# Performance work log

Hardware: AMD Instinct MI355X
Metric: run time of the kernel (lower is better)

Reference implementation:

```python
import jax, jax.numpy as jnp
import numpy as np

N = 50000
D = 256
S = 25  # num_samples


def setup_inputs() -> dict:
    key = jax.random.key(0)
    ks = jax.random.split(key, 8)
    sc = 1.0 / np.sqrt(D)
    sc2 = 1.0 / np.sqrt(2 * D)
    return {
        "features": jax.random.normal(ks[0], (N, D), dtype=jnp.float32),
        "neigh_idx": jax.random.randint(ks[1], (N, S), 0, N, dtype=jnp.int64),
        "Wp0": jax.random.normal(ks[2], (D, D), dtype=jnp.float32) * sc,
        "bp0": jnp.zeros((D,), dtype=jnp.float32),
        "Wfc0": jax.random.normal(ks[3], (2 * D, D), dtype=jnp.float32) * sc2,
        "bfc0": jnp.zeros((D,), dtype=jnp.float32),
        "Wp1": jax.random.normal(ks[4], (D, D), dtype=jnp.float32) * sc,
        "bp1": jnp.zeros((D,), dtype=jnp.float32),
        "Wfc1": jax.random.normal(ks[5], (2 * D, D), dtype=jnp.float32) * sc2,
        "bfc1": jnp.zeros((D,), dtype=jnp.float32),
    }


def _sage_layer(out, neigh_idx, Wp, bp, Wfc, bfc):
    # MaxPoolAggregator: per-node Linear+ReLU on neighbor feats, then max-pool.
    # Transform once over all nodes, then gather (same math, less traffic).
    h = jax.nn.relu(out @ Wp + bp)          # [N, d]
    agg = jnp.max(h[neigh_idx], axis=1)     # gather [N, S, d] -> max -> [N, d]
    cat = jnp.concatenate([out, agg], axis=1)  # [N, 2d]
    return cat @ Wfc + bfc                  # [N, hidden]


def reference(features, neigh_idx, Wp0, bp0, Wfc0, bfc0, Wp1, bp1, Wfc1, bfc1):
    out = _sage_layer(features, neigh_idx, Wp0, bp0, Wfc0, bfc0)
    out = jax.nn.relu(out)  # relu between layers; dropout(p=0) is a no-op
    out = _sage_layer(out, neigh_idx, Wp1, bp1, Wfc1, bfc1)
    return out
```

## Files before the change

kernel.cpp:

```cpp
#include <hip/hip_runtime.h>
#include <stdint.h>

#define N_NODES 50000
#define DD 256
#define SS 25

typedef unsigned short u16;
typedef __attribute__((ext_vector_type(8))) __bf16 bf16x8;
typedef __attribute__((ext_vector_type(4))) float f32x4;

__device__ __forceinline__ u16 f2bf(float f) {
    union { float f; uint32_t i; } c;
    c.f = f;
    uint32_t r = c.i + 0x7fffu + ((c.i >> 16) & 1u);
    return (u16)(r >> 16);
}

__device__ __forceinline__ uint4 pkmax4(uint4 a, uint4 b) {
    uint4 d;
    asm("v_pk_max_i16 %0, %1, %2" : "=v"(d.x) : "v"(a.x), "v"(b.x));
    asm("v_pk_max_i16 %0, %1, %2" : "=v"(d.y) : "v"(a.y), "v"(b.y));
    asm("v_pk_max_i16 %0, %1, %2" : "=v"(d.z) : "v"(a.z), "v"(b.z));
    asm("v_pk_max_i16 %0, %1, %2" : "=v"(d.w) : "v"(a.w), "v"(b.w));
    return d;
}

__device__ __forceinline__ void gld16(void* lds, const void* g) {
    __builtin_amdgcn_global_load_lds(
        (const __attribute__((address_space(1))) uint32_t*)g,
        (__attribute__((address_space(3))) uint32_t*)lds, 16, 0, 0);
}

__global__ __launch_bounds__(256) void cvt_f32_bf16_k(const float4* __restrict__ in,
                                                      u16* __restrict__ out) {
    int i = blockIdx.x * 256 + threadIdx.x;
    float4 v = in[i];
    uint2 o;
    o.x = (uint32_t)f2bf(v.x) | ((uint32_t)f2bf(v.y) << 16);
    o.y = (uint32_t)f2bf(v.z) | ((uint32_t)f2bf(v.w) << 16);
    *reinterpret_cast<uint2*>(out + (size_t)i * 4) = o;
}

__global__ __launch_bounds__(256) void cvt_w_k(const float* __restrict__ W,
                                               u16* __restrict__ out, int KT) {
    int t = blockIdx.x * 256 + threadIdx.x;
    if (t >= KT * 16 * 64) return;
    int lane = t & 63;
    int ct = (t >> 6) & 15;
    int kt = t >> 10;
    int k0 = kt * 32 + (lane >> 4) * 8;
    int col = ct * 16 + (lane & 15);
    u16 r[8];
#pragma unroll
    for (int e = 0; e < 8; e++) r[e] = f2bf(W[(size_t)(k0 + e) * DD + col]);
    uint4 v;
    v.x = (uint32_t)r[0] | ((uint32_t)r[1] << 16);
    v.y = (uint32_t)r[2] | ((uint32_t)r[3] << 16);
    v.z = (uint32_t)r[4] | ((uint32_t)r[5] << 16);
    v.w = (uint32_t)r[6] | ((uint32_t)r[7] << 16);
    *reinterpret_cast<uint4*>(out + (size_t)t * 8) = v;
}

__global__ __launch_bounds__(256) void gather_xcd_k(const u16* __restrict__ hc,
                                                    const int* __restrict__ idx,
                                                    u16* __restrict__ aggc, int M) {
    const int c = blockIdx.x & 7;
    const int base = (blockIdx.x >> 3) * 256;
    __shared__ int soff[256 * SS];
    const int tid = threadIdx.x;
    for (int j = tid; j < 256 * SS; j += 256) {
        int n = base + j / SS;
        if (n >= M) n = M - 1;
        soff[j] = idx[(size_t)n * SS + (j % SS)] * 32;
    }
    __syncthreads();
    const int q = tid & 3;
    const u16* slice = hc + (size_t)c * ((size_t)N_NODES * 32) + q * 8;
    u16* aslice = aggc + (size_t)c * ((size_t)N_NODES * 32) + q * 8;
#pragma unroll 1
    for (int p = 0; p < 4; ++p) {
        const int slot = p * 64 + (tid >> 2);
        const int n = base + slot;
        const int* off = &soff[slot * SS];
        uint4 v[13];
#pragma unroll
        for (int s = 0; s < 13; ++s)
            v[s] = *reinterpret_cast<const uint4*>(slice + off[s]);
        uint4 run = v[0];
#pragma unroll
        for (int s = 1; s < 13; ++s) run = pkmax4(run, v[s]);
#pragma unroll
        for (int s = 13; s < 25; ++s)
            v[s - 13] = *reinterpret_cast<const uint4*>(slice + off[s]);
#pragma unroll
        for (int s = 0; s < 12; ++s) run = pkmax4(run, v[s]);
        if (n < M)
            *reinterpret_cast<uint4*>(aslice + (size_t)n * 32) = run;
    }
}

template <int KT, bool RELU, int OMODE>
__global__ __launch_bounds__(512, 4) void gemm_k(const u16* __restrict__ A1,
                                                 const u16* __restrict__ A2,
                                                 const u16* __restrict__ Bf,
                                                 const float* __restrict__ bias,
                                                 u16* __restrict__ obf,
                                                 float* __restrict__ of32, int M) {
    __shared__ u16 sA[3][4096];
    __shared__ u16 sB[3][8192];
    const int tid = threadIdx.x;
    const int lane = tid & 63, w = tid >> 6;
    const int wm = w >> 2, wn = w & 3;
    const int row_base = blockIdx.x * 128;
    const int lr = lane & 15, lk = lane >> 4;
    const int arow = tid & 127, alk = tid >> 7;

    auto stage = [&](int buf, int kt) {
        int row = row_base + arow;
        if (row >= M) row = M - 1;
        const u16* srcA = (KT == 16 && kt >= 8)
                              ? A2 + ((size_t)(kt & 7) * N_NODES + row) * 32 + alk * 8
                              : A1 + (size_t)row * DD + (kt & 7) * 32 + alk * 8;
        gld16(&sA[buf][tid * 8], srcA);
#pragma unroll
        for (int j = 0; j < 2; ++j) {
            const int idx = tid + j * 512;
            const int nl = idx >> 6, li = idx & 63;
            gld16(&sB[buf][idx * 8], Bf + ((size_t)(kt * 16 + nl) * 64 + li) * 8);
        }
    };

    f32x4 acc[4][4] = {};
    auto compute = [&](int buf) {
        bf16x8 a[4], b[4];
#pragma unroll
        for (int m = 0; m < 4; m++)
            a[m] = *reinterpret_cast<const bf16x8*>(
                &sA[buf][(lk * 128 + wm * 64 + m * 16 + lr) * 8]);
#pragma unroll
        for (int n = 0; n < 4; n++)
            b[n] = *reinterpret_cast<const bf16x8*>(
                &sB[buf][((wn * 4 + n) * 64 + lane) * 8]);
#pragma unroll
        for (int m = 0; m < 4; m++)
#pragma unroll
            for (int n = 0; n < 4; n++)
                acc[m][n] = __builtin_amdgcn_mfma_f32_16x16x32_bf16(a[m], b[n], acc[m][n], 0, 0, 0);
    };

    stage(0, 0);
    stage(1, 1);
#pragma unroll
    for (int kt = 0; kt < KT; ++kt) {
        if (kt + 1 < KT)
            asm volatile("s_waitcnt vmcnt(3)" ::: "memory");
        else
            asm volatile("s_waitcnt vmcnt(0)" ::: "memory");
        __builtin_amdgcn_s_barrier();
        if (kt + 2 < KT) stage((kt + 2) % 3, kt + 2);
        compute(kt % 3);
    }

#pragma unroll
    for (int n = 0; n < 4; n++) {
        const int col = wn * 64 + n * 16 + lr;
        const float bz = bias[col];
#pragma unroll
        for (int m = 0; m < 4; m++) {
            const int r0 = row_base + wm * 64 + m * 16 + lk * 4;
#pragma unroll
            for (int e = 0; e < 4; e++) {
                const int r = r0 + e;
                if (r < M) {
                    float v = acc[m][n][e] + bz;
                    if (RELU) v = fmaxf(v, 0.0f);
                    if (OMODE == 0)
                        obf[(size_t)r * DD + col] = f2bf(v);
                    else if (OMODE == 1)
                        obf[((size_t)(col >> 5) * N_NODES + r) * 32 + (col & 31)] = f2bf(v);
                    else
                        of32[(size_t)r * DD + col] = v;
                }
            }
        }
    }
}

extern "C" void kernel_launch(void* const* d_in, const int* in_sizes, int n_in,
                              void* d_out, int out_size, void* d_ws, size_t ws_size,
                              hipStream_t stream) {
    const float* features = (const float*)d_in[0];
    const int* neigh = (const int*)d_in[1];
    const float* Wp0 = (const float*)d_in[2];
    const float* bp0 = (const float*)d_in[3];
    const float* Wfc0 = (const float*)d_in[4];
    const float* bfc0 = (const float*)d_in[5];
    const float* Wp1 = (const float*)d_in[6];
    const float* bp1 = (const float*)d_in[7];
    const float* Wfc1 = (const float*)d_in[8];
    const float* bfc1 = (const float*)d_in[9];
    float* out = (float*)d_out;

    const size_t ND = (size_t)N_NODES * DD;
    u16* B0 = (u16*)d_ws;
    u16* B1 = B0 + ND;
    u16* B2 = B1 + ND;
    u16* Wpb0 = B2 + ND;
    u16* Wfb0 = Wpb0 + 65536;
    u16* Wpb1 = Wfb0 + 131072;
    u16* Wfb1 = Wpb1 + 65536;

    cvt_w_k<<<32, 256, 0, stream>>>(Wp0, Wpb0, 8);
    cvt_w_k<<<64, 256, 0, stream>>>(Wfc0, Wfb0, 16);
    cvt_w_k<<<32, 256, 0, stream>>>(Wp1, Wpb1, 8);
    cvt_w_k<<<64, 256, 0, stream>>>(Wfc1, Wfb1, 16);
    cvt_f32_bf16_k<<<12500, 256, 0, stream>>>((const float4*)features, B0);

    const int gg = (N_NODES + 127) / 128;
    const int gx = ((N_NODES + 255) / 256) * 8;

    gemm_k<8, true, 1><<<gg, 512, 0, stream>>>(B0, nullptr, Wpb0, bp0, B1, nullptr, N_NODES);
    gather_xcd_k<<<gx, 256, 0, stream>>>(B1, neigh, B2, N_NODES);
    gemm_k<16, true, 0><<<gg, 512, 0, stream>>>(B0, B2, Wfb0, bfc0, B1, nullptr, N_NODES);

    gemm_k<8, true, 1><<<gg, 512, 0, stream>>>(B1, nullptr, Wpb1, bp1, B0, nullptr, N_NODES);
    gather_xcd_k<<<gx, 256, 0, stream>>>(B0, neigh, B2, N_NODES);
    gemm_k<16, false, 2><<<gg, 512, 0, stream>>>(B1, B2, Wfb1, bfc1, nullptr, out, N_NODES);
}
```

Baseline: 228.7 us.

## Deepen A-tile prefetch to four stages and make the A loads row-contiguous with an XOR swizzle

The GEMM kernel now prefetches the A tile three k-steps ahead using four LDS buffers, while B keeps its two-ahead, three-buffer pipeline. The vmcnt wait counts are adjusted to match the uneven stage depths. The A global load is rearranged so each group of four threads reads contiguous 16-byte chunks of one row, and an XOR swizzle on the chunk index keeps the LDS fragment reads free of bank conflicts. This aims to hide gather-like A load latency and improve coalescing, at the cost of extra LDS and more fragile waitcnt accounting.

```diff
diff --git a/kernel.cpp b/kernel.cpp
--- a/kernel.cpp
+++ b/kernel.cpp
@@ -106,22 +106,21 @@
                                                  const float* __restrict__ bias,
                                                  u16* __restrict__ obf,
                                                  float* __restrict__ of32, int M) {
-    __shared__ u16 sA[3][4096];
+    __shared__ u16 sA[4][4096];
     __shared__ u16 sB[3][8192];
     const int tid = threadIdx.x;
     const int lane = tid & 63, w = tid >> 6;
     const int wm = w >> 2, wn = w & 3;
     const int row_base = blockIdx.x * 128;
     const int lr = lane & 15, lk = lane >> 4;
-    const int arow = tid & 127, alk = tid >> 7;
-
-    auto stage = [&](int buf, int kt) {
-        int row = row_base + arow;
-        if (row >= M) row = M - 1;
-        const u16* srcA = (KT == 16 && kt >= 8)
-                              ? A2 + ((size_t)(kt & 7) * N_NODES + row) * 32 + alk * 8
-                              : A1 + (size_t)row * DD + (kt & 7) * 32 + alk * 8;
-        gld16(&sA[buf][tid * 8], srcA);
+
+    const int arow = tid >> 2;
+    const int swzr = (arow + (arow >> 2)) & 3;
+    const int kc = (tid & 3) ^ swzr;
+    int sgrow = row_base + arow;
+    if (sgrow >= M) sgrow = M - 1;
+
+    auto stageB = [&](int buf, int kt) {
 #pragma unroll
         for (int j = 0; j < 2; ++j) {
             const int idx = tid + j * 512;
@@ -129,18 +128,27 @@
             gld16(&sB[buf][idx * 8], Bf + ((size_t)(kt * 16 + nl) * 64 + li) * 8);
         }
     };
+    auto stageA = [&](int buf, int kt) {
+        const u16* srcA = (KT == 16 && kt >= 8)
+                              ? A2 + ((size_t)(kt & 7) * N_NODES + sgrow) * 32 + kc * 8
+                              : A1 + (size_t)sgrow * DD + (kt & 7) * 32 + kc * 8;
+        gld16(&sA[buf][tid * 8], srcA);
+    };
 
     f32x4 acc[4][4] = {};
-    auto compute = [&](int buf) {
+    const int swzl = (lr + (lr >> 2)) & 3;
+    auto compute = [&](int bufA, int bufB) {
         bf16x8 a[4], b[4];
 #pragma unroll
-        for (int m = 0; m < 4; m++)
+        for (int m = 0; m < 4; m++) {
+            const int row = wm * 64 + m * 16 + lr;
             a[m] = *reinterpret_cast<const bf16x8*>(
-                &sA[buf][(lk * 128 + wm * 64 + m * 16 + lr) * 8]);
+                &sA[bufA][(row * 4 + (lk ^ swzl)) * 8]);
+        }
 #pragma unroll
         for (int n = 0; n < 4; n++)
             b[n] = *reinterpret_cast<const bf16x8*>(
-                &sB[buf][((wn * 4 + n) * 64 + lane) * 8]);
+                &sB[bufB][((wn * 4 + n) * 64 + lane) * 8]);
 #pragma unroll
         for (int m = 0; m < 4; m++)
 #pragma unroll
@@ -148,17 +156,23 @@
                 acc[m][n] = __builtin_amdgcn_mfma_f32_16x16x32_bf16(a[m], b[n], acc[m][n], 0, 0, 0);
     };
 
-    stage(0, 0);
-    stage(1, 1);
+    stageB(0, 0);
+    stageA(0, 0);
+    stageB(1, 1);
+    stageA(1, 1);
+    stageA(2, 2);
 #pragma unroll
     for (int kt = 0; kt < KT; ++kt) {
-        if (kt + 1 < KT)
+        if (kt < KT - 2)
+            asm volatile("s_waitcnt vmcnt(4)" ::: "memory");
+        else if (kt == KT - 2)
             asm volatile("s_waitcnt vmcnt(3)" ::: "memory");
         else
             asm volatile("s_waitcnt vmcnt(0)" ::: "memory");
         __builtin_amdgcn_s_barrier();
-        if (kt + 2 < KT) stage((kt + 2) % 3, kt + 2);
-        compute(kt % 3);
+        if (kt + 2 < KT) stageB((kt + 2) % 3, kt + 2);
+        if (kt + 3 < KT) stageA((kt + 3) & 3, kt + 3);
+        compute(kt & 3, kt % 3);
     }
 
 #pragma unroll
```

Result: faster. 221.9 us (-3.0%).
